# Kernel tuning notes

Hardware: AMD Instinct MI355X
Metric: run time of the kernel (lower is better)

Reference implementation:

```python
import jax, jax.numpy as jnp
import numpy as np

H = 2048      # hidden_dim
NH = 32       # num_heads
HD = H // NH  # head_dim


def setup_inputs() -> dict:
    key = jax.random.key(0)
    ks = jax.random.split(key, 9)
    s = 1.0 / np.sqrt(H)
    return {
        "hidden_states": jax.random.normal(ks[0], (2, 2048, H), dtype=jnp.float32),
        "wq": jax.random.uniform(ks[1], (H, H), jnp.float32, -s, s),
        "bq": jnp.zeros((H,), jnp.float32),
        "wk": jax.random.uniform(ks[2], (H, H), jnp.float32, -s, s),
        "bk": jnp.zeros((H,), jnp.float32),
        "wv": jax.random.uniform(ks[3], (H, H), jnp.float32, -s, s),
        "bv": jnp.zeros((H,), jnp.float32),
        "wo": jax.random.uniform(ks[4], (H, H), jnp.float32, -s, s),
        "bo": jnp.zeros((H,), jnp.float32),
    }


def reference(hidden_states, wq, bq, wk, bk, wv, bv, wo, bo):
    B, S, _ = hidden_states.shape
    def heads(x):  # [B,S,H] -> [B,NH,S,HD]
        return x.reshape(B, S, NH, HD).transpose(0, 2, 1, 3)
    q = heads(hidden_states @ wq.T + bq)
    k = heads(hidden_states @ wk.T + bk)
    v = heads(hidden_states @ wv.T + bv)
    scores = jnp.einsum("bhqd,bhkd->bhqk", q, k) / np.sqrt(HD).astype(np.float32)
    causal = jnp.tril(jnp.ones((S, S), dtype=bool))
    scores = jnp.where(causal, scores, -jnp.inf)
    attn = jax.nn.softmax(scores, axis=-1)
    out = jnp.einsum("bhqk,bhkd->bhqd", attn, v)
    out = out.transpose(0, 2, 1, 3).reshape(B, S, H)
    return out @ wo.T + bo
```

## Files before the change

kernel.cpp:

```cpp
#include <hip/hip_runtime.h>
#include <hip/hip_bf16.h>

#define HDIM 2048
#define NHEADS 32
#define HEADD 64
#define NBATCH 2
#define SEQLEN 2048
#define MTOT (NBATCH * SEQLEN)
#define NQT (SEQLEN / 128)
#define LDQKV 6144

typedef __bf16 bf16;
typedef __bf16 bf16x8 __attribute__((ext_vector_type(8)));
typedef float f32x4 __attribute__((ext_vector_type(4)));
typedef float f32x8 __attribute__((ext_vector_type(8)));
typedef float f32x16 __attribute__((ext_vector_type(16)));

__device__ __forceinline__ void gload_lds16(const bf16* g, bf16* l) {
  __builtin_amdgcn_global_load_lds(
      (const __attribute__((address_space(1))) void*)g,
      (__attribute__((address_space(3))) void*)l, 16, 0, 0);
}

__device__ __forceinline__ unsigned cvtpk_bf16(float lo, float hi) {
  unsigned r;
  asm("v_cvt_pk_bf16_f32 %0, %1, %2" : "=v"(r) : "v"(lo), "v"(hi));
  return r;
}

__device__ __forceinline__ float max3f(float a, float b, float c) {
  float r;
  asm("v_max3_f32 %0, %1, %2, %3" : "=v"(r) : "v"(a), "v"(b), "v"(c));
  return r;
}

__global__ void __launch_bounds__(256) cvt_f32_to_bf16(
    const float* __restrict__ src, bf16* __restrict__ dst, int n) {
  int i = (blockIdx.x * 256 + threadIdx.x) * 8;
  if (i >= n) return;
  f32x8 a = *(const f32x8*)(src + i);
  bf16x8 o;
#pragma unroll
  for (int j = 0; j < 8; ++j) o[j] = (bf16)a[j];
  *(bf16x8*)(dst + i) = o;
}

__global__ void __launch_bounds__(256) cvt4_f32_to_bf16(
    const float* __restrict__ s0, const float* __restrict__ s1,
    const float* __restrict__ s2, const float* __restrict__ s3,
    bf16* __restrict__ d0, bf16* __restrict__ d1,
    bf16* __restrict__ d2, bf16* __restrict__ d3) {
  const float* src; bf16* dst;
  switch (blockIdx.y) {
    case 0: src = s0; dst = d0; break;
    case 1: src = s1; dst = d1; break;
    case 2: src = s2; dst = d2; break;
    default: src = s3; dst = d3; break;
  }
  int i = (blockIdx.x * 256 + threadIdx.x) * 8;
  f32x8 a = *(const f32x8*)(src + i);
  bf16x8 o;
#pragma unroll
  for (int j = 0; j < 8; ++j) o[j] = (bf16)a[j];
  *(bf16x8*)(dst + i) = o;
}

__global__ void __launch_bounds__(256) pack_bias(
    const float* __restrict__ bq, const float* __restrict__ bk,
    const float* __restrict__ bv, float* __restrict__ out) {
  int i = blockIdx.x * 256 + threadIdx.x;
  if (i >= LDQKV) return;
  float v;
  if (i < HDIM) v = bq[i];
  else if (i < 2 * HDIM) v = bk[i - HDIM];
  else v = bv[i - 2 * HDIM];
  out[i] = v;
}

template <int BM, bool OUT_F32>
__global__ void __launch_bounds__(512, 2) gemm3(
    const bf16* __restrict__ A, const bf16* __restrict__ W,
    const float* __restrict__ bias, void* __restrict__ Cout,
    int Ndim, float scale) {
  constexpr int NT = 64;
  constexpr int FM = BM / 32;
  constexpr int NPH = FM / 4;
  constexpr int ALD = BM / 128;
  constexpr int LPT = ALD + 2;
  constexpr int MPX = (4096 / BM) / 8;
  __shared__ bf16 As[4][BM * 32];
  __shared__ bf16 Bs[4][256 * 32];

  const int tid = threadIdx.x;
  const int l = tid & 63;
  const int w = tid >> 6;
  const int wm = w >> 2;
  const int wn = w & 3;

  const int wid = blockIdx.x;
  const int j = wid >> 3;
  const int m0 = ((wid & 7) * MPX + (j & (MPX - 1))) * BM;
  const int n0 = (j / MPX) * 256;

  const float secsc = (n0 < 2048) ? scale : 1.0f;

  const int rowA = tid >> 2;
  const int cg = (((tid & 3) ^ ((tid >> 3) & 3))) * 8;

  auto stageA = [&](int s, int kt) {
    const int k0 = kt * 32 + cg;
#pragma unroll
    for (int i = 0; i < ALD; ++i)
      gload_lds16(A + (size_t)(m0 + i * 128 + rowA) * 2048 + k0,
                  &As[s][(i * 512 + w * 64) * 8]);
  };
  auto stageB = [&](int s, int kt) {
    const int k0 = kt * 32 + cg;
#pragma unroll
    for (int i = 0; i < 2; ++i)
      gload_lds16(W + (size_t)(n0 + i * 128 + rowA) * 2048 + k0,
                  &Bs[s][(i * 512 + w * 64) * 8]);
  };

  f32x4 acc[FM][4];
#pragma unroll
  for (int mf = 0; mf < FM; ++mf)
#pragma unroll
    for (int nf = 0; nf < 4; ++nf) acc[mf][nf] = {0.f, 0.f, 0.f, 0.f};

  const int fr = l & 15;
  const int fch = (((l >> 4) ^ ((fr >> 1) & 3))) * 8;

  stageA(0, 0); stageB(0, 0);
  stageA(1, 1); stageB(1, 1);
  stageA(2, 2); stageB(2, 2);
  if constexpr (LPT == 4)
    asm volatile("s_waitcnt vmcnt(8)" ::: "memory");
  else
    asm volatile("s_waitcnt vmcnt(6)" ::: "memory");
  __builtin_amdgcn_s_barrier();

  for (int t = 0; t < NT; ++t) {
    const int s = t & 3;
    const int sn = (t + 3) & 3;
    const bool st = (t + 3) < NT;

    bf16x8 bf0[4], af0[4];
#pragma unroll
    for (int nf = 0; nf < 4; ++nf)
      bf0[nf] = *(const bf16x8*)&Bs[s][(wn * 64 + nf * 16 + fr) * 32 + fch];
#pragma unroll
    for (int f = 0; f < 4; ++f)
      af0[f] = *(const bf16x8*)&As[s][(wm * (BM / 2) + f * 16 + fr) * 32 + fch];
    if (st) stageA(sn, t + 3);
    if constexpr (NPH == 1) {
      if (st) stageB(sn, t + 3);
      if (t < NT - 3)
        asm volatile("s_waitcnt vmcnt(6)" ::: "memory");
      else if (t == NT - 3)
        asm volatile("s_waitcnt vmcnt(3)" ::: "memory");
      else
        asm volatile("s_waitcnt vmcnt(0)" ::: "memory");
    }
    __builtin_amdgcn_s_barrier();
    __builtin_amdgcn_s_setprio(1);
#pragma unroll
    for (int f = 0; f < 4; ++f)
#pragma unroll
      for (int nf = 0; nf < 4; ++nf)
        acc[f][nf] = __builtin_amdgcn_mfma_f32_16x16x32_bf16(
            af0[f], bf0[nf], acc[f][nf], 0, 0, 0);
    __builtin_amdgcn_s_setprio(0);
    __builtin_amdgcn_s_barrier();

    if constexpr (NPH == 2) {
      bf16x8 af1[4];
#pragma unroll
      for (int f = 0; f < 4; ++f)
        af1[f] = *(const bf16x8*)&As[s]
            [(wm * (BM / 2) + (4 + f) * 16 + fr) * 32 + fch];
      if (st) stageB(sn, t + 3);
      if (t < NT - 3)
        asm volatile("s_waitcnt vmcnt(8)" ::: "memory");
      else if (t == NT - 3)
        asm volatile("s_waitcnt vmcnt(4)" ::: "memory");
      else
        asm volatile("s_waitcnt vmcnt(0)" ::: "memory");
      __builtin_amdgcn_s_barrier();
      __builtin_amdgcn_s_setprio(1);
#pragma unroll
      for (int f = 0; f < 4; ++f)
#pragma unroll
        for (int nf = 0; nf < 4; ++nf)
          acc[4 + f][nf] = __builtin_amdgcn_mfma_f32_16x16x32_bf16(
              af1[f], bf0[nf], acc[4 + f][nf], 0, 0, 0);
      __builtin_amdgcn_s_setprio(0);
      __builtin_amdgcn_s_barrier();
    }
  }

  const int rj = (l >> 4) * 4;
#pragma unroll
  for (int mf = 0; mf < FM; ++mf)
#pragma unroll
    for (int nf = 0; nf < 4; ++nf) {
      const int col = n0 + wn * 64 + nf * 16 + fr;
      const float bvl = bias[col];
#pragma unroll
      for (int jj = 0; jj < 4; ++jj) {
        const int row = m0 + wm * (BM / 2) + mf * 16 + rj + jj;
        const float v = (acc[mf][nf][jj] + bvl) * secsc;
        if constexpr (OUT_F32)
          ((float*)Cout)[(size_t)row * Ndim + col] = v;
        else
          ((bf16*)Cout)[(size_t)row * Ndim + col] = (bf16)v;
      }
    }
}

__global__ void __launch_bounds__(256) transpose_v(
    const bf16* __restrict__ QKV, bf16* __restrict__ Vt) {
  __shared__ bf16 T[64][72];
  const int t = threadIdx.x;
  const int s0 = blockIdx.x * 64;
  const int h = blockIdx.y, b = blockIdx.z;
  const size_t inb = (size_t)b * SEQLEN * LDQKV + 2 * HDIM + (size_t)h * HEADD;
#pragma unroll
  for (int i = 0; i < 2; ++i) {
    const int idx = t + i * 256;
    const int r = idx >> 3, c = (idx & 7) * 8;
    *(bf16x8*)&T[r][c] = *(const bf16x8*)&QKV[inb + (size_t)(s0 + r) * LDQKV + c];
  }
  __syncthreads();
  const size_t outb = (size_t)(b * NHEADS + h) * HEADD * SEQLEN + s0;
#pragma unroll
  for (int i = 0; i < 2; ++i) {
    const int idx = t + i * 256;
    const int d = idx >> 3, cs = (idx & 7) * 8;
    bf16x8 o;
#pragma unroll
    for (int j = 0; j < 8; ++j) o[j] = T[cs + j][d];
    *(bf16x8*)&Vt[outb + (size_t)d * SEQLEN + cs] = o;
  }
}

__global__ void __launch_bounds__(256) attn4(
    const bf16* __restrict__ QKV, const bf16* __restrict__ Vt,
    bf16* __restrict__ O) {
  __shared__ bf16 Kl[2][64 * 64];
  __shared__ bf16 Vl[2][64 * 64];

  const int tid = threadIdx.x;
  const int l = tid & 63;
  const int w = tid >> 6;
  const int lq = l & 31;
  const int g = l >> 5;
  const int h = blockIdx.y, b = blockIdx.z;
  const size_t baseQ = (size_t)b * SEQLEN * LDQKV + (size_t)h * HEADD;
  const size_t baseK = baseQ + HDIM;
  const size_t baseV = (size_t)(b * NHEADS + h) * HEADD * SEQLEN;
  const size_t baseO = (size_t)b * SEQLEN * HDIM + (size_t)h * HEADD;

  const int L0 = w * 128 + l;
  const int L1 = w * 128 + 64 + l;
  const int r0 = L0 >> 3, gc0 = ((L0 & 7) ^ (r0 & 7)) * 8;
  const int r1 = L1 >> 3, gc1 = ((L1 & 7) ^ (r1 & 7)) * 8;
  const int dst0 = (w * 128) * 8;
  const int dst1 = (w * 128 + 64) * 8;

  auto stage = [&](int bufi, int kt) {
    const int k0s = kt * 64;
    gload_lds16(QKV + baseK + (size_t)(k0s + r0) * LDQKV + gc0, &Kl[bufi][dst0]);
    gload_lds16(QKV + baseK + (size_t)(k0s + r1) * LDQKV + gc1, &Kl[bufi][dst1]);
    gload_lds16(Vt + baseV + (size_t)r0 * SEQLEN + k0s + gc0, &Vl[bufi][dst0]);
    gload_lds16(Vt + baseV + (size_t)r1 * SEQLEN + k0s + gc1, &Vl[bufi][dst1]);
  };

#pragma unroll
  for (int seg = 0; seg < 2; ++seg) {
    const int qt = seg ? blockIdx.x : (NQT - 1 - blockIdx.x);
    const int q0 = qt * 128;
    const int qw = q0 + w * 32;
    const int qa = qw + lq;

    bf16x8 qf[4];
#pragma unroll
    for (int ks = 0; ks < 4; ++ks)
      qf[ks] = *(const bf16x8*)&QKV[baseQ + (size_t)qa * LDQKV + ks * 16 + g * 8];

    f32x16 oacc0, oacc1;
#pragma unroll
    for (int r = 0; r < 16; ++r) { oacc0[r] = 0.f; oacc1[r] = 0.f; }
    float mrun = -__builtin_inff(), lrun = 0.f;

    const int nkt = q0 / 64 + 2;
    stage(0, 0);

    for (int kt = 0; kt < nkt; ++kt) {
      const int cur = kt & 1;
      const int k0 = kt * 64;
      if (kt + 1 < nkt) {
        stage(cur ^ 1, kt + 1);
        asm volatile("s_waitcnt vmcnt(4)" ::: "memory");
      } else {
        asm volatile("s_waitcnt vmcnt(0)" ::: "memory");
      }
      __builtin_amdgcn_s_barrier();

      if (k0 <= qw + 31) {
        f32x16 st0, st1;
#pragma unroll
        for (int r = 0; r < 16; ++r) { st0[r] = 0.f; st1[r] = 0.f; }
        __builtin_amdgcn_s_setprio(1);
#pragma unroll
        for (int ks = 0; ks < 4; ++ks) {
          const int cr = (((2 * ks + g) ^ (lq & 7))) * 8;
          bf16x8 kf0 = *(const bf16x8*)&Kl[cur][lq * 64 + cr];
          bf16x8 kf1 = *(const bf16x8*)&Kl[cur][(32 + lq) * 64 + cr];
          st0 = __builtin_amdgcn_mfma_f32_32x32x16_bf16(kf0, qf[ks], st0, 0, 0, 0);
          st1 = __builtin_amdgcn_mfma_f32_32x32x16_bf16(kf1, qf[ks], st1, 0, 0, 0);
        }
        __builtin_amdgcn_s_setprio(0);

        if (k0 + 63 > qw) {
#pragma unroll
          for (int r = 0; r < 16; ++r) {
            const int ro = (r & 3) + 8 * (r >> 2) + 4 * g;
            if (k0 + ro > qa) st0[r] = -__builtin_inff();
            if (k0 + 32 + ro > qa) st1[r] = -__builtin_inff();
          }
        }

        float mx[8];
#pragma unroll
        for (int r = 0; r < 8; ++r)
          mx[r] = fmaxf(max3f(st0[r], st0[r + 8], st1[r]), st1[r + 8]);
        const float ma = max3f(mx[0], mx[1], mx[2]);
        const float mb = max3f(mx[3], mx[4], mx[5]);
        const float mc = max3f(mx[6], mx[7], ma);
        const float mtree = fmaxf(mb, mc);
        const float pm = fmaxf(mtree, __shfl_xor(mtree, 32));

        const float mnew = fmaxf(mrun, pm);
        if (!__all(pm - mrun <= 11.0f)) {
          const float sc = __builtin_amdgcn_exp2f(mrun - mnew);
          lrun *= sc;
#pragma unroll
          for (int r = 0; r < 16; ++r) {
            const int ro = (r & 3) + 8 * (r >> 2) + 4 * g;
            const float scr = __shfl(sc, ro);
            oacc0[r] *= scr;
            oacc1[r] *= scr;
          }
          mrun = mnew;
        }

#pragma unroll
        for (int r = 0; r < 16; ++r) {
          st0[r] = __builtin_amdgcn_exp2f(st0[r] - mrun);
          st1[r] = __builtin_amdgcn_exp2f(st1[r] - mrun);
        }
        float sm[8];
#pragma unroll
        for (int r = 0; r < 8; ++r)
          sm[r] = (st0[r] + st0[r + 8]) + (st1[r] + st1[r + 8]);
#pragma unroll
        for (int s = 4; s > 0; s >>= 1)
#pragma unroll
          for (int r = 0; r < 4; ++r)
            if (r < s) sm[r] += sm[r + s];
        lrun += sm[0] + __shfl_xor(sm[0], 32);

        unsigned wd0[8], wd1[8];
#pragma unroll
        for (int i = 0; i < 8; ++i) {
          wd0[i] = cvtpk_bf16(st0[2 * i], st0[2 * i + 1]);
          wd1[i] = cvtpk_bf16(st1[2 * i], st1[2 * i + 1]);
        }
        bf16x8 paf[4];
#pragma unroll
        for (int kt2 = 0; kt2 < 2; ++kt2)
#pragma unroll
          for (int hf = 0; hf < 2; ++hf) {
            const unsigned* wsrc = kt2 ? wd1 : wd0;
            const unsigned a0 = wsrc[hf * 4 + 0], a1 = wsrc[hf * 4 + 1];
            const unsigned b0 = wsrc[hf * 4 + 2], b1 = wsrc[hf * 4 + 3];
            const unsigned sb0 = (unsigned)__shfl_xor((int)b0, 32);
            const unsigned sb1 = (unsigned)__shfl_xor((int)b1, 32);
            const unsigned sa0 = (unsigned)__shfl_xor((int)a0, 32);
            const unsigned sa1 = (unsigned)__shfl_xor((int)a1, 32);
            union { unsigned u[4]; bf16x8 v; } fu;
            fu.u[0] = g ? sb0 : a0;
            fu.u[1] = g ? sb1 : a1;
            fu.u[2] = g ? b0 : sa0;
            fu.u[3] = g ? b1 : sa1;
            paf[kt2 * 2 + hf] = fu.v;
          }

        __builtin_amdgcn_s_setprio(1);
#pragma unroll
        for (int s = 0; s < 4; ++s) {
          const int cr = (((2 * s + g) ^ (lq & 7))) * 8;
          bf16x8 vf0 = *(const bf16x8*)&Vl[cur][lq * 64 + cr];
          bf16x8 vf1 = *(const bf16x8*)&Vl[cur][(32 + lq) * 64 + cr];
          oacc0 = __builtin_amdgcn_mfma_f32_32x32x16_bf16(paf[s], vf0, oacc0, 0, 0, 0);
          oacc1 = __builtin_amdgcn_mfma_f32_32x32x16_bf16(paf[s], vf1, oacc1, 0, 0, 0);
        }
        __builtin_amdgcn_s_setprio(0);
      }
      __builtin_amdgcn_s_barrier();
    }

#pragma unroll
    for (int r = 0; r < 16; ++r) {
      const int ro = (r & 3) + 8 * (r >> 2) + 4 * g;
      const float lr = __shfl(lrun, ro);
      const float inv = 1.0f / lr;
      O[baseO + (size_t)(qw + ro) * HDIM + lq] = (bf16)(oacc0[r] * inv);
      O[baseO + (size_t)(qw + ro) * HDIM + 32 + lq] = (bf16)(oacc1[r] * inv);
    }
  }
}

extern "C" void kernel_launch(void* const* d_in, const int* in_sizes, int n_in,
                              void* d_out, int out_size, void* d_ws, size_t ws_size,
                              hipStream_t stream) {
  (void)in_sizes; (void)n_in; (void)out_size; (void)ws_size;
  const float* hs = (const float*)d_in[0];
  const float* wq = (const float*)d_in[1];
  const float* bq = (const float*)d_in[2];
  const float* wk = (const float*)d_in[3];
  const float* bk = (const float*)d_in[4];
  const float* wv = (const float*)d_in[5];
  const float* bv = (const float*)d_in[6];
  const float* wo = (const float*)d_in[7];
  const float* bo = (const float*)d_in[8];

  char* wsp = (char*)d_ws;
  bf16* hsb  = (bf16*)wsp; wsp += (size_t)MTOT * HDIM * sizeof(bf16);
  bf16* wqb  = (bf16*)wsp; wsp += (size_t)HDIM * HDIM * sizeof(bf16);
  bf16* wkb  = (bf16*)wsp; wsp += (size_t)HDIM * HDIM * sizeof(bf16);
  bf16* wvb  = (bf16*)wsp; wsp += (size_t)HDIM * HDIM * sizeof(bf16);
  bf16* wob  = (bf16*)wsp; wsp += (size_t)HDIM * HDIM * sizeof(bf16);
  bf16* QKVb = (bf16*)wsp; wsp += (size_t)MTOT * LDQKV * sizeof(bf16);
  float* biasqkv = (float*)wsp; wsp += (size_t)LDQKV * sizeof(float);
  bf16* aob = hsb;
  bf16* Vtb = wqb;

  const int nHS = MTOT * HDIM;
  const int nW = HDIM * HDIM;
  cvt_f32_to_bf16<<<nHS / 2048, 256, 0, stream>>>(hs, hsb, nHS);
  dim3 gc(nW / 2048, 4);
  cvt4_f32_to_bf16<<<gc, 256, 0, stream>>>(wq, wk, wv, wo, wqb, wkb, wvb, wob);
  pack_bias<<<LDQKV / 256, 256, 0, stream>>>(bq, bk, bv, biasqkv);

  gemm3<256, false><<<dim3(16 * (LDQKV / 256)), 512, 0, stream>>>(
      hsb, wqb, biasqkv, QKVb, LDQKV, 0.125f * 1.44269504f);

  dim3 gt(SEQLEN / 64, NHEADS, NBATCH);
  transpose_v<<<gt, 256, 0, stream>>>(QKVb, Vtb);

  dim3 ga(NQT / 2, NHEADS, NBATCH);
  attn4<<<ga, 256, 0, stream>>>(QKVb, Vtb, aob);

  gemm3<128, true><<<dim3(32 * (HDIM / 256)), 512, 0, stream>>>(
      aob, wob, bo, (float*)d_out, HDIM, 1.0f);
}
```

Measured before the change: 275.7 us.

## Collapse GEMM k-loop phases into one barrier per iteration

The projection GEMM main loop is restructured. Each step now loads all A and B fragments, issues the prefetch for both tiles, runs all MFMAs, then waits on the outstanding global loads and hits a single workgroup barrier. Previously the loop used two to four barriers per step and split the BM=256 case into two MFMA phases. The aim is to cut barrier stalls and let more MFMAs overlap with the in-flight loads, at the cost of keeping all A fragments live in registers at once, which raises register pressure for the larger tile.

```diff
diff --git a/kernel.cpp b/kernel.cpp
--- a/kernel.cpp
+++ b/kernel.cpp
@@ -84,7 +84,6 @@
     int Ndim, float scale) {
   constexpr int NT = 64;
   constexpr int FM = BM / 32;
-  constexpr int NPH = FM / 4;
   constexpr int ALD = BM / 128;
   constexpr int LPT = ALD + 2;
   constexpr int MPX = (4096 / BM) / 8;
@@ -145,58 +144,39 @@
     const int sn = (t + 3) & 3;
     const bool st = (t + 3) < NT;
 
-    bf16x8 bf0[4], af0[4];
+    bf16x8 bf[4], af[FM];
 #pragma unroll
     for (int nf = 0; nf < 4; ++nf)
-      bf0[nf] = *(const bf16x8*)&Bs[s][(wn * 64 + nf * 16 + fr) * 32 + fch];
-#pragma unroll
-    for (int f = 0; f < 4; ++f)
-      af0[f] = *(const bf16x8*)&As[s][(wm * (BM / 2) + f * 16 + fr) * 32 + fch];
-    if (st) stageA(sn, t + 3);
-    if constexpr (NPH == 1) {
-      if (st) stageB(sn, t + 3);
-      if (t < NT - 3)
-        asm volatile("s_waitcnt vmcnt(6)" ::: "memory");
-      else if (t == NT - 3)
-        asm volatile("s_waitcnt vmcnt(3)" ::: "memory");
-      else
-        asm volatile("s_waitcnt vmcnt(0)" ::: "memory");
-    }
-    __builtin_amdgcn_s_barrier();
+      bf[nf] = *(const bf16x8*)&Bs[s][(wn * 64 + nf * 16 + fr) * 32 + fch];
+#pragma unroll
+    for (int f = 0; f < FM; ++f)
+      af[f] = *(const bf16x8*)&As[s][(wm * (BM / 2) + f * 16 + fr) * 32 + fch];
+
+    if (st) { stageA(sn, t + 3); stageB(sn, t + 3); }
+
     __builtin_amdgcn_s_setprio(1);
 #pragma unroll
-    for (int f = 0; f < 4; ++f)
+    for (int f = 0; f < FM; ++f)
 #pragma unroll
       for (int nf = 0; nf < 4; ++nf)
         acc[f][nf] = __builtin_amdgcn_mfma_f32_16x16x32_bf16(
-            af0[f], bf0[nf], acc[f][nf], 0, 0, 0);
+            af[f], bf[nf], acc[f][nf], 0, 0, 0);
     __builtin_amdgcn_s_setprio(0);
-    __builtin_amdgcn_s_barrier();
-
-    if constexpr (NPH == 2) {
-      bf16x8 af1[4];
-#pragma unroll
-      for (int f = 0; f < 4; ++f)
-        af1[f] = *(const bf16x8*)&As[s]
-            [(wm * (BM / 2) + (4 + f) * 16 + fr) * 32 + fch];
-      if (st) stageB(sn, t + 3);
-      if (t < NT - 3)
+
+    if (t < NT - 3) {
+      if constexpr (LPT == 4)
         asm volatile("s_waitcnt vmcnt(8)" ::: "memory");
-      else if (t == NT - 3)
+      else
+        asm volatile("s_waitcnt vmcnt(6)" ::: "memory");
+    } else if (t == NT - 3) {
+      if constexpr (LPT == 4)
         asm volatile("s_waitcnt vmcnt(4)" ::: "memory");
       else
-        asm volatile("s_waitcnt vmcnt(0)" ::: "memory");
-      __builtin_amdgcn_s_barrier();
-      __builtin_amdgcn_s_setprio(1);
-#pragma unroll
-      for (int f = 0; f < 4; ++f)
-#pragma unroll
-        for (int nf = 0; nf < 4; ++nf)
-          acc[4 + f][nf] = __builtin_amdgcn_mfma_f32_16x16x32_bf16(
-              af1[f], bf0[nf], acc[4 + f][nf], 0, 0, 0);
-      __builtin_amdgcn_s_setprio(0);
-      __builtin_amdgcn_s_barrier();
+        asm volatile("s_waitcnt vmcnt(3)" ::: "memory");
+    } else if (t == NT - 2) {
+      asm volatile("s_waitcnt vmcnt(0)" ::: "memory");
     }
+    if (t < NT - 1) __builtin_amdgcn_s_barrier();
   }
 
   const int rj = (l >> 4) * 4;
```

Result: faster. 262.7 us (-4.7%).
